# Kernel tuning notes

Measured on AMD Instinct MI355X. Metric: run time of the kernel, lower is better.

The kernel has to match this reference:

```python
import jax, jax.numpy as jnp
import numpy as np

EPS = 1e-12  # keras K.l2_normalize epsilon


def _l2_normalize(v, axis):
    return v * jax.lax.rsqrt(jnp.maximum(jnp.sum(v * v, axis=axis, keepdims=True), EPS))


def setup_inputs() -> dict:
    key = jax.random.key(0)
    k1, k2, k3, k4 = jax.random.split(key, 4)
    B, T, D, K, O = 32, 1024, 512, 64, 1024
    x = jax.random.normal(k1, (B, T, D), dtype=jnp.float32)
    weight = jax.random.normal(k2, (D, K), dtype=jnp.float32) * (1.0 / np.sqrt(D))
    bias = jnp.zeros((K,), dtype=jnp.float32)
    centers = jax.random.normal(k3, (K, D), dtype=jnp.float32)
    reduc_dim = jax.random.normal(k4, (D * K, O), dtype=jnp.float32) * 0.01
    return {"x": x, "weight": weight, "bias": bias, "centers": centers, "reduc_dim": reduc_dim}


def reference(x, weight, bias, centers, reduc_dim):
    # x: [B,T,D], weight: [D,K], bias: [K]
    # soft assignment: softmax over centers
    a = jax.nn.softmax(jnp.einsum('btd,dk->btk', x, weight) + bias, axis=-1)  # [B,T,K]
    # aggregate descriptors per center: batch_dot over time axis -> [B,K,D]
    x_agg = jnp.einsum('btk,btd->bkd', a, x)
    # total soft weight per center: [B,K]
    sum_w = jnp.sum(a, axis=1)
    # residual vs centers, broadcast: [B,K,D]
    full = x_agg - sum_w[:, :, None] * centers[None, :, :]
    # intra-normalize per center vector
    full = _l2_normalize(full, axis=-1)
    B = x.shape[0]
    full = full.reshape(B, -1)  # [B, K*D]
    full = _l2_normalize(full, axis=-1)
    return full @ reduc_dim  # [B, output_dim]
```

## Files before the change

### kernel.cpp

```cpp
#include <hip/hip_runtime.h>
#include <math.h>

#define TT 1024
#define DD 512
#define KK 64
#define OO 1024
#define EPSF 1e-12f

typedef __attribute__((ext_vector_type(8))) short bf16x8;
typedef __attribute__((ext_vector_type(4))) float f32x4;

__device__ __forceinline__ ushort f2bf(float f) {
  unsigned u = __float_as_uint(f);
  u = (u + 0x7FFFu + ((u >> 16) & 1u)) >> 16;
  return (ushort)u;
}
__device__ __forceinline__ float bf2f(ushort h) {
  return __uint_as_float(((unsigned)h) << 16);
}


__global__ __launch_bounds__(256) void nv_k0(const float* __restrict__ w,
                                             ushort* __restrict__ whT,
                                             float* __restrict__ sum_w) {
  int idx = blockIdx.x * 256 + threadIdx.x;
  if (idx < 32768) {
    int d = idx >> 6, k = idx & 63;
    whT[(size_t)k * DD + d] = f2bf(w[idx]);
  } else if (idx < 32768 + 2048) {
    sum_w[idx - 32768] = 0.f;
  }
}

__global__ __launch_bounds__(512) void nv_k12(
    const float* __restrict__ x, const ushort* __restrict__ whT,
    const float* __restrict__ bias, float* __restrict__ xaggP,
    float* __restrict__ sum_w) {
  const int tsp = blockIdx.x, b = blockIdx.y;
  const int t0 = tsp * 128;
  const int tid = threadIdx.x;
  const int wave = tid >> 6, lane = tid & 63, l15 = lane & 15, q = lane >> 4;

  __shared__ ushort xT[512 * 128];
  __shared__ ushort xsa[128 * 64];
  __shared__ ushort wsm[64 * 64];
  ushort* xs = xsa;
  ushort* aTl = xsa;

  f32x4 acc[4];
#pragma unroll
  for (int nt = 0; nt < 4; ++nt)
#pragma unroll
    for (int r = 0; r < 4; ++r) acc[nt][r] = 0.f;

  for (int dc = 0; dc < DD; dc += 64) {
#pragma unroll
    for (int it = 0; it < 2; ++it) {
      int gi = it * 512 + tid;
      int t = gi >> 3, gd = gi & 7;
      const float* px = x + (size_t)(b * TT + t0 + t) * DD + dc + gd * 8;
      float4 v0 = *(const float4*)px;
      float4 v1 = *(const float4*)(px + 4);
      bf16x8 pk;
      pk[0] = (short)f2bf(v0.x); pk[1] = (short)f2bf(v0.y);
      pk[2] = (short)f2bf(v0.z); pk[3] = (short)f2bf(v0.w);
      pk[4] = (short)f2bf(v1.x); pk[5] = (short)f2bf(v1.y);
      pk[6] = (short)f2bf(v1.z); pk[7] = (short)f2bf(v1.w);
      *(bf16x8*)(xs + t * 64 + ((gd ^ (t & 7)) << 3)) = pk;
      const int tg = t >> 3, tlo = t & 7;
#pragma unroll
      for (int j = 0; j < 8; ++j) {
        const int d = dc + gd * 8 + j;
        xT[d * 128 + ((tg ^ (d & 15)) << 3) + tlo] = (ushort)pk[j];
      }
    }
    {
      int k = tid >> 3, gd = tid & 7;
      bf16x8 v = *(const bf16x8*)(whT + (size_t)k * DD + dc + gd * 8);
      *(bf16x8*)(wsm + k * 64 + ((gd ^ (k & 7)) << 3)) = v;
    }
    __syncthreads();
#pragma unroll
    for (int kc = 0; kc < 2; ++kc) {
      const int gq = kc * 4 + q;
      bf16x8 bfv[4];
#pragma unroll
      for (int nt = 0; nt < 4; ++nt) {
        const int k = nt * 16 + l15;
        bfv[nt] = *(const bf16x8*)(wsm + k * 64 + ((gq ^ (k & 7)) << 3));
      }
      const int t = wave * 16 + l15;
      bf16x8 af = *(const bf16x8*)(xs + t * 64 + ((gq ^ (t & 7)) << 3));
#pragma unroll
      for (int nt = 0; nt < 4; ++nt)
        acc[nt] = __builtin_amdgcn_mfma_f32_16x16x32_bf16(af, bfv[nt], acc[nt], 0, 0, 0);
    }
    __syncthreads();
  }

  float bia[4];
#pragma unroll
  for (int nt = 0; nt < 4; ++nt) bia[nt] = bias[nt * 16 + l15];

  ushort au[4][4];
  float sw[4] = {0.f, 0.f, 0.f, 0.f};
#pragma unroll
  for (int r = 0; r < 4; ++r) {
    float l[4];
#pragma unroll
    for (int nt = 0; nt < 4; ++nt) l[nt] = acc[nt][r] + bia[nt];
    float m = fmaxf(fmaxf(l[0], l[1]), fmaxf(l[2], l[3]));
#pragma unroll
    for (int s = 1; s <= 8; s <<= 1) m = fmaxf(m, __shfl_xor(m, s));
    float e[4];
#pragma unroll
    for (int nt = 0; nt < 4; ++nt) e[nt] = __expf(l[nt] - m);
    float ssum = e[0] + e[1] + e[2] + e[3];
#pragma unroll
    for (int s = 1; s <= 8; s <<= 1) ssum += __shfl_xor(ssum, s);
    float inv = 1.f / ssum;
#pragma unroll
    for (int nt = 0; nt < 4; ++nt) {
      ushort u = f2bf(e[nt] * inv);
      au[nt][r] = u;
      sw[nt] += bf2f(u);
    }
  }
#pragma unroll
  for (int nt = 0; nt < 4; ++nt) {
    float s = sw[nt];
    s += __shfl_xor(s, 16);
    s += __shfl_xor(s, 32);
    if (q == 0) atomicAdd(sum_w + b * KK + nt * 16 + l15, s);
  }

  __syncthreads();
#pragma unroll
  for (int nt = 0; nt < 4; ++nt)
#pragma unroll
    for (int r = 0; r < 4; ++r) {
      const int k = nt * 16 + l15;
      const int t = wave * 16 + q * 4 + r;
      aTl[k * 128 + (((t >> 3) ^ (k & 15)) << 3) + (t & 7)] = au[nt][r];
    }
  __syncthreads();

  f32x4 accB[4][4];
#pragma unroll
  for (int mk = 0; mk < 4; ++mk)
#pragma unroll
    for (int nd = 0; nd < 4; ++nd)
#pragma unroll
      for (int r = 0; r < 4; ++r) accB[mk][nd][r] = 0.f;

#pragma unroll
  for (int kc = 0; kc < 4; ++kc) {
    const int g = kc * 4 + q;
    bf16x8 afr[4], bfr[4];
#pragma unroll
    for (int mk = 0; mk < 4; ++mk) {
      const int k = mk * 16 + l15;
      afr[mk] = *(const bf16x8*)(aTl + k * 128 + ((g ^ (k & 15)) << 3));
    }
#pragma unroll
    for (int nd = 0; nd < 4; ++nd) {
      const int d = wave * 64 + nd * 16 + l15;
      bfr[nd] = *(const bf16x8*)(xT + d * 128 + ((g ^ (d & 15)) << 3));
    }
#pragma unroll
    for (int mk = 0; mk < 4; ++mk)
#pragma unroll
      for (int nd = 0; nd < 4; ++nd)
        accB[mk][nd] =
            __builtin_amdgcn_mfma_f32_16x16x32_bf16(afr[mk], bfr[nd], accB[mk][nd], 0, 0, 0);
  }
#pragma unroll
  for (int mk = 0; mk < 4; ++mk)
#pragma unroll
    for (int nd = 0; nd < 4; ++nd)
#pragma unroll
      for (int r = 0; r < 4; ++r) {
        const int k = mk * 16 + q * 4 + r;
        const int d = wave * 64 + nd * 16 + l15;
        xaggP[(size_t)((tsp * 32 + b) * KK + k) * DD + d] = accB[mk][nd][r];
      }
}

__global__ __launch_bounds__(128) void nv_k3a(
    const float* __restrict__ xaggP, float* __restrict__ full,
    const float* __restrict__ centers, const float* __restrict__ sum_w,
    float* __restrict__ s1) {
  const int k = blockIdx.x, b = blockIdx.y;
  const int tid = threadIdx.x;
  const float sw = sum_w[b * KK + k];
  float4 v = make_float4(0.f, 0.f, 0.f, 0.f);
#pragma unroll
  for (int sp = 0; sp < 8; ++sp) {
    float4 p = *((const float4*)(xaggP + (size_t)((sp * 32 + b) * KK + k) * DD) + tid);
    v.x += p.x; v.y += p.y; v.z += p.z; v.w += p.w;
  }
  float4 c = *((const float4*)(centers + (size_t)k * DD) + tid);
  v.x = fmaf(-sw, c.x, v.x);
  v.y = fmaf(-sw, c.y, v.y);
  v.z = fmaf(-sw, c.z, v.z);
  v.w = fmaf(-sw, c.w, v.w);
  *((float4*)(full + (size_t)(b * KK + k) * DD) + tid) = v;
  float ss = v.x * v.x + v.y * v.y + v.z * v.z + v.w * v.w;
#pragma unroll
  for (int s = 1; s <= 32; s <<= 1) ss += __shfl_xor(ss, s);
  __shared__ float red[2];
  if ((tid & 63) == 0) red[tid >> 6] = ss;
  __syncthreads();
  if (tid == 0) s1[b * KK + k] = red[0] + red[1];
}

__global__ __launch_bounds__(256) void nv_k3c(const float* __restrict__ full,
                                              const float* __restrict__ s1,
                                              float* __restrict__ fullT) {
  const int k = blockIdx.x, d0 = blockIdx.y * 128;
  const int tid = threadIdx.x;
  __shared__ float ls[32 * 132];
  __shared__ float s2s[32];

  {
    int bb = tid >> 3, k8 = tid & 7;
    float p = 0.f;
#pragma unroll
    for (int i = 0; i < 8; ++i) {
      float r = s1[bb * KK + k8 * 8 + i];
      p += r / fmaxf(r, EPSF);
    }
    p += __shfl_xor(p, 1);
    p += __shfl_xor(p, 2);
    p += __shfl_xor(p, 4);
    if (k8 == 0) s2s[bb] = rsqrtf(fmaxf(p, EPSF));
  }
  __syncthreads();

#pragma unroll
  for (int it = 0; it < 4; ++it) {
    int fi = it * 256 + tid;
    int b = fi >> 5, dg = fi & 31;
    float r = s1[b * KK + k];
    float sc = rsqrtf(fmaxf(r, EPSF)) * s2s[b];
    float4 v = *((const float4*)(full + (size_t)(b * KK + k) * DD + d0) + dg);
    v.x *= sc; v.y *= sc; v.z *= sc; v.w *= sc;
    *(float4*)(ls + b * 132 + dg * 4) = v;
  }
  __syncthreads();
#pragma unroll
  for (int it = 0; it < 4; ++it) {
    int fo = it * 256 + tid;
    int d = fo >> 3, bq = fo & 7;
    float4 v;
    v.x = ls[(bq * 4 + 0) * 132 + d];
    v.y = ls[(bq * 4 + 1) * 132 + d];
    v.z = ls[(bq * 4 + 2) * 132 + d];
    v.w = ls[(bq * 4 + 3) * 132 + d];
    *(float4*)(fullT + (size_t)(k * DD + d0 + d) * 32 + bq * 4) = v;
  }
}

__global__ __launch_bounds__(256) void nv_k4(
    const float* __restrict__ fullT, const float* __restrict__ reduc,
    float* __restrict__ outP) {
  const int strip = blockIdx.x;
  const int ksp = blockIdx.y;
  const int tid = threadIdx.x;
  const int wave = tid >> 6, lane = tid & 63;
  const int c0 = strip * 256 + lane * 4;
  const int kblk = ksp * 256;

  __shared__ float fst[256 * 32];

#pragma unroll
  for (int it = 0; it < 8; ++it) {
    int f4 = it * 256 + tid;
    *(float4*)(fst + f4 * 4) = *(const float4*)(fullT + (size_t)kblk * 32 + f4 * 4);
  }
  __syncthreads();

  float4 acc[32];
#pragma unroll
  for (int b = 0; b < 32; ++b) acc[b] = make_float4(0.f, 0.f, 0.f, 0.f);

  const int kw = wave * 64;
  for (int kk = 0; kk < 64; kk += 4) {
    float4 rv[4];
#pragma unroll
    for (int j = 0; j < 4; ++j)
      rv[j] = *(const float4*)(reduc + (size_t)(kblk + kw + kk + j) * OO + c0);
#pragma unroll
    for (int j = 0; j < 4; ++j) {
      const int kl = kw + kk + j;
#pragma unroll
      for (int b4 = 0; b4 < 8; ++b4) {
        float4 fv = *(const float4*)(fst + kl * 32 + b4 * 4);
        acc[b4 * 4 + 0].x = fmaf(fv.x, rv[j].x, acc[b4 * 4 + 0].x);
        acc[b4 * 4 + 0].y = fmaf(fv.x, rv[j].y, acc[b4 * 4 + 0].y);
        acc[b4 * 4 + 0].z = fmaf(fv.x, rv[j].z, acc[b4 * 4 + 0].z);
        acc[b4 * 4 + 0].w = fmaf(fv.x, rv[j].w, acc[b4 * 4 + 0].w);
        acc[b4 * 4 + 1].x = fmaf(fv.y, rv[j].x, acc[b4 * 4 + 1].x);
        acc[b4 * 4 + 1].y = fmaf(fv.y, rv[j].y, acc[b4 * 4 + 1].y);
        acc[b4 * 4 + 1].z = fmaf(fv.y, rv[j].z, acc[b4 * 4 + 1].z);
        acc[b4 * 4 + 1].w = fmaf(fv.y, rv[j].w, acc[b4 * 4 + 1].w);
        acc[b4 * 4 + 2].x = fmaf(fv.z, rv[j].x, acc[b4 * 4 + 2].x);
        acc[b4 * 4 + 2].y = fmaf(fv.z, rv[j].y, acc[b4 * 4 + 2].y);
        acc[b4 * 4 + 2].z = fmaf(fv.z, rv[j].z, acc[b4 * 4 + 2].z);
        acc[b4 * 4 + 2].w = fmaf(fv.z, rv[j].w, acc[b4 * 4 + 2].w);
        acc[b4 * 4 + 3].x = fmaf(fv.w, rv[j].x, acc[b4 * 4 + 3].x);
        acc[b4 * 4 + 3].y = fmaf(fv.w, rv[j].y, acc[b4 * 4 + 3].y);
        acc[b4 * 4 + 3].z = fmaf(fv.w, rv[j].z, acc[b4 * 4 + 3].z);
        acc[b4 * 4 + 3].w = fmaf(fv.w, rv[j].w, acc[b4 * 4 + 3].w);
      }
    }
  }

  __syncthreads();
  for (int w = 0; w < 4; ++w) {
    if (wave == w) {
      if (w == 0) {
#pragma unroll
        for (int b = 0; b < 32; ++b)
          *(float4*)(fst + b * 256 + lane * 4) = acc[b];
      } else {
#pragma unroll
        for (int b = 0; b < 32; ++b) {
          float4 v = *(float4*)(fst + b * 256 + lane * 4);
          v.x += acc[b].x; v.y += acc[b].y; v.z += acc[b].z; v.w += acc[b].w;
          *(float4*)(fst + b * 256 + lane * 4) = v;
        }
      }
    }
    __syncthreads();
  }

#pragma unroll
  for (int it = 0; it < 8; ++it) {
    int f4 = it * 256 + tid;
    int b = f4 >> 6, cg = f4 & 63;
    *(float4*)(outP + ((size_t)(ksp * 32 + b) * OO) + strip * 256 + cg * 4) =
        *(const float4*)(fst + b * 256 + cg * 4);
  }
}

__global__ __launch_bounds__(128) void nv_k5(const float* __restrict__ outP,
                                             float* __restrict__ out) {
  const int idx = blockIdx.x * 128 + threadIdx.x;
  float s = 0.f;
#pragma unroll 8
  for (int sp = 0; sp < 128; ++sp) s += outP[(size_t)sp * 32768 + idx];
  out[idx] = s;
}

extern "C" void kernel_launch(void* const* d_in, const int* in_sizes, int n_in,
                              void* d_out, int out_size, void* d_ws, size_t ws_size,
                              hipStream_t stream) {
  const float* x = (const float*)d_in[0];
  const float* weight = (const float*)d_in[1];
  const float* bias = (const float*)d_in[2];
  const float* centers = (const float*)d_in[3];
  const float* reduc = (const float*)d_in[4];
  float* out = (float*)d_out;
  float* ws = (float*)d_ws;

  float* xaggP = ws;
  float* full = ws + 8388608;
  float* fullT = ws + 9437184;
  float* outP = ws + 10485760;
  ushort* whT = (ushort*)(ws + 14680064);
  float* sum_w = ws + 14696448;
  float* s1 = sum_w + 2048;

  nv_k0<<<136, 256, 0, stream>>>(weight, whT, sum_w);
  nv_k12<<<dim3(8, 32), 512, 0, stream>>>(x, whT, bias, xaggP, sum_w);
  nv_k3a<<<dim3(64, 32), 128, 0, stream>>>(xaggP, full, centers, sum_w, s1);
  nv_k3c<<<dim3(64, 4), 256, 0, stream>>>(full, s1, fullT);
  nv_k4<<<dim3(4, 128), 256, 0, stream>>>(fullT, reduc, outP);
  nv_k5<<<256, 128, 0, stream>>>(outP, out);
}
```

Before: 275.2 us.

## Use split-bf16 MFMA for final projection GEMM and drop transpose kernel

Replaces the scalar-FMA final GEMM (full @ reduc_dim) with MFMA bf16 16x16x32 instructions, using a hi/lo bf16 split (three products) to keep accuracy close to fp32. The transpose/normalize kernel is replaced by a tiny kernel that computes per-(b,k) scale factors, and the scale is applied while staging A tiles into swizzled LDS. The K-split shrinks from 128 to 32 partials, which reduces the partial-sum reduction traffic. The risks are the bf16 split error and lower occupancy per block.

```diff
diff --git a/kernel.cpp b/kernel.cpp
--- a/kernel.cpp
+++ b/kernel.cpp
@@ -204,7 +204,7 @@
   v.y = fmaf(-sw, c.y, v.y);
   v.z = fmaf(-sw, c.z, v.z);
   v.w = fmaf(-sw, c.w, v.w);
-  *((float4*)(full + (size_t)(b * KK + k) * DD) + tid) = v;
+  *((float4*)(full + (size_t)b * (KK * DD) + (size_t)k * DD) + tid) = v;
   float ss = v.x * v.x + v.y * v.y + v.z * v.z + v.w * v.w;
 #pragma unroll
   for (int s = 1; s <= 32; s <<= 1) ss += __shfl_xor(ss, s);
@@ -214,134 +214,124 @@
   if (tid == 0) s1[b * KK + k] = red[0] + red[1];
 }
 
-__global__ __launch_bounds__(256) void nv_k3c(const float* __restrict__ full,
-                                              const float* __restrict__ s1,
-                                              float* __restrict__ fullT) {
-  const int k = blockIdx.x, d0 = blockIdx.y * 128;
-  const int tid = threadIdx.x;
-  __shared__ float ls[32 * 132];
-  __shared__ float s2s[32];
-
-  {
-    int bb = tid >> 3, k8 = tid & 7;
-    float p = 0.f;
-#pragma unroll
-    for (int i = 0; i < 8; ++i) {
-      float r = s1[bb * KK + k8 * 8 + i];
-      p += r / fmaxf(r, EPSF);
-    }
-    p += __shfl_xor(p, 1);
-    p += __shfl_xor(p, 2);
-    p += __shfl_xor(p, 4);
-    if (k8 == 0) s2s[bb] = rsqrtf(fmaxf(p, EPSF));
-  }
-  __syncthreads();
-
-#pragma unroll
-  for (int it = 0; it < 4; ++it) {
-    int fi = it * 256 + tid;
-    int b = fi >> 5, dg = fi & 31;
-    float r = s1[b * KK + k];
-    float sc = rsqrtf(fmaxf(r, EPSF)) * s2s[b];
-    float4 v = *((const float4*)(full + (size_t)(b * KK + k) * DD + d0) + dg);
-    v.x *= sc; v.y *= sc; v.z *= sc; v.w *= sc;
-    *(float4*)(ls + b * 132 + dg * 4) = v;
-  }
-  __syncthreads();
-#pragma unroll
-  for (int it = 0; it < 4; ++it) {
-    int fo = it * 256 + tid;
-    int d = fo >> 3, bq = fo & 7;
-    float4 v;
-    v.x = ls[(bq * 4 + 0) * 132 + d];
-    v.y = ls[(bq * 4 + 1) * 132 + d];
-    v.z = ls[(bq * 4 + 2) * 132 + d];
-    v.w = ls[(bq * 4 + 3) * 132 + d];
-    *(float4*)(fullT + (size_t)(k * DD + d0 + d) * 32 + bq * 4) = v;
-  }
+__global__ __launch_bounds__(64) void nv_k3b(const float* __restrict__ s1,
+                                             float* __restrict__ scale) {
+  const int b = blockIdx.x, k = threadIdx.x;
+  float r = s1[b * KK + k];
+  float d1 = fmaxf(r, EPSF);
+  float s2 = r / d1;
+#pragma unroll
+  for (int s = 1; s <= 32; s <<= 1) s2 += __shfl_xor(s2, s);
+  scale[b * KK + k] = rsqrtf(d1) * rsqrtf(fmaxf(s2, EPSF));
 }
 
 __global__ __launch_bounds__(256) void nv_k4(
-    const float* __restrict__ fullT, const float* __restrict__ reduc,
-    float* __restrict__ outP) {
-  const int strip = blockIdx.x;
+    const float* __restrict__ full, const float* __restrict__ scale,
+    const float* __restrict__ reduc, float* __restrict__ outP) {
+  const int osp = blockIdx.x;
   const int ksp = blockIdx.y;
   const int tid = threadIdx.x;
-  const int wave = tid >> 6, lane = tid & 63;
-  const int c0 = strip * 256 + lane * 4;
-  const int kblk = ksp * 256;
-
-  __shared__ float fst[256 * 32];
-
-#pragma unroll
-  for (int it = 0; it < 8; ++it) {
-    int f4 = it * 256 + tid;
-    *(float4*)(fst + f4 * 4) = *(const float4*)(fullT + (size_t)kblk * 32 + f4 * 4);
-  }
-  __syncthreads();
-
-  float4 acc[32];
-#pragma unroll
-  for (int b = 0; b < 32; ++b) acc[b] = make_float4(0.f, 0.f, 0.f, 0.f);
-
-  const int kw = wave * 64;
-  for (int kk = 0; kk < 64; kk += 4) {
-    float4 rv[4];
-#pragma unroll
-    for (int j = 0; j < 4; ++j)
-      rv[j] = *(const float4*)(reduc + (size_t)(kblk + kw + kk + j) * OO + c0);
-#pragma unroll
-    for (int j = 0; j < 4; ++j) {
-      const int kl = kw + kk + j;
-#pragma unroll
-      for (int b4 = 0; b4 < 8; ++b4) {
-        float4 fv = *(const float4*)(fst + kl * 32 + b4 * 4);
-        acc[b4 * 4 + 0].x = fmaf(fv.x, rv[j].x, acc[b4 * 4 + 0].x);
-        acc[b4 * 4 + 0].y = fmaf(fv.x, rv[j].y, acc[b4 * 4 + 0].y);
-        acc[b4 * 4 + 0].z = fmaf(fv.x, rv[j].z, acc[b4 * 4 + 0].z);
-        acc[b4 * 4 + 0].w = fmaf(fv.x, rv[j].w, acc[b4 * 4 + 0].w);
-        acc[b4 * 4 + 1].x = fmaf(fv.y, rv[j].x, acc[b4 * 4 + 1].x);
-        acc[b4 * 4 + 1].y = fmaf(fv.y, rv[j].y, acc[b4 * 4 + 1].y);
-        acc[b4 * 4 + 1].z = fmaf(fv.y, rv[j].z, acc[b4 * 4 + 1].z);
-        acc[b4 * 4 + 1].w = fmaf(fv.y, rv[j].w, acc[b4 * 4 + 1].w);
-        acc[b4 * 4 + 2].x = fmaf(fv.z, rv[j].x, acc[b4 * 4 + 2].x);
-        acc[b4 * 4 + 2].y = fmaf(fv.z, rv[j].y, acc[b4 * 4 + 2].y);
-        acc[b4 * 4 + 2].z = fmaf(fv.z, rv[j].z, acc[b4 * 4 + 2].z);
-        acc[b4 * 4 + 2].w = fmaf(fv.z, rv[j].w, acc[b4 * 4 + 2].w);
-        acc[b4 * 4 + 3].x = fmaf(fv.w, rv[j].x, acc[b4 * 4 + 3].x);
-        acc[b4 * 4 + 3].y = fmaf(fv.w, rv[j].y, acc[b4 * 4 + 3].y);
-        acc[b4 * 4 + 3].z = fmaf(fv.w, rv[j].z, acc[b4 * 4 + 3].z);
-        acc[b4 * 4 + 3].w = fmaf(fv.w, rv[j].w, acc[b4 * 4 + 3].w);
-      }
-    }
-  }
-
-  __syncthreads();
-  for (int w = 0; w < 4; ++w) {
-    if (wave == w) {
-      if (w == 0) {
-#pragma unroll
-        for (int b = 0; b < 32; ++b)
-          *(float4*)(fst + b * 256 + lane * 4) = acc[b];
-      } else {
-#pragma unroll
-        for (int b = 0; b < 32; ++b) {
-          float4 v = *(float4*)(fst + b * 256 + lane * 4);
-          v.x += acc[b].x; v.y += acc[b].y; v.z += acc[b].z; v.w += acc[b].w;
-          *(float4*)(fst + b * 256 + lane * 4) = v;
-        }
-      }
-    }
+  const int wave = tid >> 6, lane = tid & 63, l15 = lane & 15, q = lane >> 4;
+  const int ob = osp * 64;
+  const int r00 = ksp * 1024;
+
+  __shared__ ushort rTh[64 * 64];
+  __shared__ ushort rTl[64 * 64];
+  __shared__ ushort ahs[32 * 64];
+  __shared__ ushort als[32 * 64];
+  __shared__ float scs[64];
+
+  if (tid < 64) scs[tid] = scale[(tid & 31) * KK + ksp * 2 + (tid >> 5)];
+
+  const int Br = tid >> 2, Bo = (tid & 3) * 16;
+  const int Bg = Br >> 3, Be = Br & 7;
+  const int Ab = tid >> 3, Ak = (tid & 7) * 8;
+  const int Asl = ((tid & 7) ^ (Ab & 7)) << 3;
+
+  const float* rbB = reduc + (size_t)(r00 + Br) * OO + ob + Bo;
+  const float* rbA = full + (size_t)Ab * 32768 + r00 + Ak;
+
+  f32x4 acc[2];
+#pragma unroll
+  for (int mt = 0; mt < 2; ++mt)
+#pragma unroll
+    for (int rr = 0; rr < 4; ++rr) acc[mt][rr] = 0.f;
+
+  float4 bv0, bv1, bv2, bv3, av0, av1;
+  bv0 = *(const float4*)(rbB + 0);
+  bv1 = *(const float4*)(rbB + 4);
+  bv2 = *(const float4*)(rbB + 8);
+  bv3 = *(const float4*)(rbB + 12);
+  av0 = *(const float4*)(rbA + 0);
+  av1 = *(const float4*)(rbA + 4);
+
+  for (int ks = 0; ks < 16; ++ks) {
     __syncthreads();
-  }
-
-#pragma unroll
-  for (int it = 0; it < 8; ++it) {
-    int f4 = it * 256 + tid;
-    int b = f4 >> 6, cg = f4 & 63;
-    *(float4*)(outP + ((size_t)(ksp * 32 + b) * OO) + strip * 256 + cg * 4) =
-        *(const float4*)(fst + b * 256 + cg * 4);
-  }
+    {
+      float vv[16] = {bv0.x, bv0.y, bv0.z, bv0.w, bv1.x, bv1.y, bv1.z, bv1.w,
+                      bv2.x, bv2.y, bv2.z, bv2.w, bv3.x, bv3.y, bv3.z, bv3.w};
+#pragma unroll
+      for (int j = 0; j < 16; ++j) {
+        const int o = Bo + j;
+        const int sl = ((Bg ^ (o & 7)) << 3) + Be;
+        float f = vv[j];
+        ushort h = f2bf(f);
+        rTh[o * 64 + sl] = h;
+        rTl[o * 64 + sl] = f2bf(f - bf2f(h));
+      }
+    }
+    {
+      const float sc = scs[Ab + ((ks >> 3) << 5)];
+      float aa[8] = {av0.x, av0.y, av0.z, av0.w, av1.x, av1.y, av1.z, av1.w};
+      bf16x8 hi, lo;
+#pragma unroll
+      for (int e = 0; e < 8; ++e) {
+        float f = aa[e] * sc;
+        ushort h = f2bf(f);
+        hi[e] = (short)h;
+        lo[e] = (short)f2bf(f - bf2f(h));
+      }
+      *(bf16x8*)(ahs + Ab * 64 + Asl) = hi;
+      *(bf16x8*)(als + Ab * 64 + Asl) = lo;
+    }
+    __syncthreads();
+    if (ks < 15) {
+      const float* pB = rbB + (size_t)(ks + 1) * 64 * OO;
+      const float* pA = rbA + (ks + 1) * 64;
+      bv0 = *(const float4*)(pB + 0);
+      bv1 = *(const float4*)(pB + 4);
+      bv2 = *(const float4*)(pB + 8);
+      bv3 = *(const float4*)(pB + 12);
+      av0 = *(const float4*)(pA + 0);
+      av1 = *(const float4*)(pA + 4);
+    }
+#pragma unroll
+    for (int kc = 0; kc < 2; ++kc) {
+      const int gq = kc * 4 + q;
+      const int o = wave * 16 + l15;
+      const int bsl = (gq ^ (o & 7)) << 3;
+      bf16x8 bh = *(const bf16x8*)(rTh + o * 64 + bsl);
+      bf16x8 bl = *(const bf16x8*)(rTl + o * 64 + bsl);
+#pragma unroll
+      for (int mt = 0; mt < 2; ++mt) {
+        const int b = mt * 16 + l15;
+        const int asl = (gq ^ (b & 7)) << 3;
+        bf16x8 ah = *(const bf16x8*)(ahs + b * 64 + asl);
+        bf16x8 al = *(const bf16x8*)(als + b * 64 + asl);
+        acc[mt] = __builtin_amdgcn_mfma_f32_16x16x32_bf16(ah, bh, acc[mt], 0, 0, 0);
+        acc[mt] = __builtin_amdgcn_mfma_f32_16x16x32_bf16(ah, bl, acc[mt], 0, 0, 0);
+        acc[mt] = __builtin_amdgcn_mfma_f32_16x16x32_bf16(al, bh, acc[mt], 0, 0, 0);
+      }
+    }
+  }
+
+#pragma unroll
+  for (int mt = 0; mt < 2; ++mt)
+#pragma unroll
+    for (int rr = 0; rr < 4; ++rr) {
+      const int b = mt * 16 + q * 4 + rr;
+      outP[(size_t)(ksp * 32 + b) * OO + ob + wave * 16 + l15] = acc[mt][rr];
+    }
 }
 
 __global__ __launch_bounds__(128) void nv_k5(const float* __restrict__ outP,
@@ -349,7 +339,7 @@
   const int idx = blockIdx.x * 128 + threadIdx.x;
   float s = 0.f;
 #pragma unroll 8
-  for (int sp = 0; sp < 128; ++sp) s += outP[(size_t)sp * 32768 + idx];
+  for (int sp = 0; sp < 32; ++sp) s += outP[(size_t)sp * 32768 + idx];
   out[idx] = s;
 }
 
@@ -366,16 +356,16 @@
 
   float* xaggP = ws;
   float* full = ws + 8388608;
-  float* fullT = ws + 9437184;
-  float* outP = ws + 10485760;
-  ushort* whT = (ushort*)(ws + 14680064);
-  float* sum_w = ws + 14696448;
+  float* outP = ws + 9437184;
+  ushort* whT = (ushort*)(ws + 10485760);
+  float* sum_w = ws + 10502144;
   float* s1 = sum_w + 2048;
+  float* scale = sum_w + 4096;
 
   nv_k0<<<136, 256, 0, stream>>>(weight, whT, sum_w);
   nv_k12<<<dim3(8, 32), 512, 0, stream>>>(x, whT, bias, xaggP, sum_w);
   nv_k3a<<<dim3(64, 32), 128, 0, stream>>>(xaggP, full, centers, sum_w, s1);
-  nv_k3c<<<dim3(64, 4), 256, 0, stream>>>(full, s1, fullT);
-  nv_k4<<<dim3(4, 128), 256, 0, stream>>>(fullT, reduc, outP);
+  nv_k3b<<<32, 64, 0, stream>>>(s1, scale);
+  nv_k4<<<dim3(16, 32), 256, 0, stream>>>(full, scale, reduc, outP);
   nv_k5<<<256, 128, 0, stream>>>(outP, out);
 }
```

Result: faster. 267.8 us (-2.7%).
